# Kernel optimization log

Measured on AMD Instinct MI355X. Metric: run time of the kernel, lower is better.

The kernel has to match this reference:

```python
import jax, jax.numpy as jnp
import numpy as np

HEAD_NUM = 12
HEAD_SIZE = 64
INPUT_DIM = 768
BATCH = 2
SEQ = 2048
NEG = 1e12


def setup_inputs() -> dict:
    key = jax.random.key(0)
    k1, k2, k3 = jax.random.split(key, 3)
    x = jax.random.normal(k1, (BATCH, SEQ, INPUT_DIM), dtype=jnp.float32)
    W = jax.random.normal(k2, (INPUT_DIM, HEAD_NUM * HEAD_SIZE * 2), dtype=jnp.float32) * 0.02
    b = jax.random.normal(k3, (HEAD_NUM * HEAD_SIZE * 2,), dtype=jnp.float32) * 0.02
    mask = jnp.ones((BATCH, SEQ), dtype=jnp.int32)
    return {"x": x, "W": W, "b": b, "mask": mask}


def _rope_tables(n, d, dtype):
    # SinusoidalPositionEmbedding(head_size, 'zero'): pos[..., 0::2]=sin, 1::2=cos
    pos = jnp.arange(n, dtype=dtype)
    freqs = jnp.power(10000.0, -2.0 * jnp.arange(d // 2, dtype=dtype) / d)
    ang = pos[:, None] * freqs[None, :]  # [n, d/2]
    # K.repeat_elements(pos[..., 1::2], 2, -1) -> each cos value repeated twice
    cos_pos = jnp.repeat(jnp.cos(ang), 2, axis=-1)  # [n, d]
    sin_pos = jnp.repeat(jnp.sin(ang), 2, axis=-1)  # [n, d]
    return cos_pos[None, :, None, :], sin_pos[None, :, None, :]  # [1,n,1,d]


def _rotate_half(t):
    # stack([-t[...,1::2], t[...,::2]], -1).reshape(t.shape)
    t2 = jnp.stack([-t[..., 1::2], t[..., 0::2]], axis=-1)
    return t2.reshape(t.shape)


def reference(x, W, b, mask):
    bsz, n, _ = x.shape
    proj = (x @ W + b).reshape(bsz, n, HEAD_NUM, 2 * HEAD_SIZE)  # [b,n,h,2d]
    qw, kw = proj[..., :HEAD_SIZE], proj[..., HEAD_SIZE:]
    cos_pos, sin_pos = _rope_tables(n, HEAD_SIZE, x.dtype)
    qw = qw * cos_pos + _rotate_half(qw) * sin_pos
    kw = kw * cos_pos + _rotate_half(kw) * sin_pos
    logits = jnp.einsum('bmhd,bnhd->bhmn', qw, kw)  # [b,h,m,n]
    m = mask.astype(logits.dtype)
    logits = logits - (1.0 - m[:, None, :, None]) * NEG  # mask query axis (dim 2)
    logits = logits - (1.0 - m[:, None, None, :]) * NEG  # mask key axis (dim 3)
    tri = jnp.triu(jnp.ones((n, n), dtype=logits.dtype))  # band_part(0,-1): keep m<=n
    logits = logits - (1.0 - tri) * NEG
    return logits / (HEAD_SIZE ** 0.5)
```

## Files before the change

kernel.cpp:

```cpp
#include <hip/hip_runtime.h>

#define SEQ    2048
#define IND    768
#define NPROJ  1536
#define BHN    24
#define NEGV   1000000000000.0f

typedef __attribute__((ext_vector_type(4))) float f32x4;
typedef __attribute__((ext_vector_type(8))) short s16x8;
typedef __attribute__((ext_vector_type(8))) unsigned short u16x8;
typedef __attribute__((ext_vector_type(4))) unsigned short u16x4;

__device__ __forceinline__ unsigned short f2bf(float f) {
  unsigned int u = __builtin_bit_cast(unsigned int, f);
  u += 0x7fffu + ((u >> 16) & 1u);
  return (unsigned short)(u >> 16);
}

__device__ __forceinline__ void nt_store4(float* p, f32x4 v) {
  __builtin_nontemporal_store(v, (f32x4*)p);
}

#define GLOAD_LDS16(g, l)                                              \
  __builtin_amdgcn_global_load_lds(                                    \
      (const __attribute__((address_space(1))) void*)(g),              \
      (__attribute__((address_space(3))) void*)(l), 16, 0, 0)

__device__ __forceinline__ void stage128x64(const unsigned short* __restrict__ src,
                                            size_t stride, int4* lds, int tid) {
  const int w = tid >> 6, l = tid & 63;
#pragma unroll
  for (int i = 0; i < 4; ++i) {
    int gb = w * 256 + i * 64;
    int G = gb + l;
    int row = G >> 3, g = G & 7;
    int cb = g ^ (row & 7);
    GLOAD_LDS16(src + (size_t)row * stride + cb * 8, lds + gb);
  }
}

__global__ __launch_bounds__(256) void k_prep(const float* __restrict__ x,
                                              const float* __restrict__ W,
                                              unsigned short* __restrict__ xb,
                                              unsigned short* __restrict__ Wt,
                                              float* __restrict__ cosT,
                                              float* __restrict__ sinT) {
  __shared__ float Ws[64][65];
  const int bid = blockIdx.x;
  const int tid = threadIdx.x;

  if (bid < 1536) {
    int i = (bid * 256 + tid) * 8;
    float4 a = *(const float4*)(x + i);
    float4 b = *(const float4*)(x + i + 4);
    u16x8 o;
    o[0] = f2bf(a.x); o[1] = f2bf(a.y); o[2] = f2bf(a.z); o[3] = f2bf(a.w);
    o[4] = f2bf(b.x); o[5] = f2bf(b.y); o[6] = f2bf(b.z); o[7] = f2bf(b.w);
    *(u16x8*)(xb + i) = o;
  } else if (bid < 1824) {
    int tb = bid - 1536;
    int nt = tb % 24, kt = tb / 24;
    int n0 = nt * 64, k0 = kt * 64;
    int cr = tid >> 4;
    int cc = (tid & 15) * 4;
#pragma unroll
    for (int it = 0; it < 4; ++it) {
      int kr = it * 16 + cr;
      float4 v = *(const float4*)(W + (size_t)(k0 + kr) * NPROJ + n0 + cc);
      Ws[kr][cc + 0] = v.x; Ws[kr][cc + 1] = v.y;
      Ws[kr][cc + 2] = v.z; Ws[kr][cc + 3] = v.w;
    }
    __syncthreads();
#pragma unroll
    for (int it = 0; it < 4; ++it) {
      int nl = it * 16 + cr;
      u16x4 o;
#pragma unroll
      for (int q = 0; q < 4; ++q) o[q] = f2bf(Ws[cc + q][nl]);
      *(u16x4*)(Wt + (size_t)(n0 + nl) * IND + k0 + cc) = o;
    }
  } else {
    int i = (bid - 1824) * 256 + tid;
    int s = i >> 5, f = i & 31;
    float freq = exp2f(-(float)f * (13.287712379549449f / 32.0f));
    float ang = (float)s * freq;
    float sv, cv;
    sincosf(ang, &sv, &cv);
    cosT[i] = cv; sinT[i] = sv;
  }
}

__global__ __launch_bounds__(256, 2) void k_proj(const unsigned short* __restrict__ xb,
                                                 const unsigned short* __restrict__ Wt,
                                                 const float* __restrict__ bias,
                                                 unsigned short* __restrict__ Qb,
                                                 unsigned short* __restrict__ Kb,
                                                 const float* __restrict__ cosT,
                                                 const float* __restrict__ sinT) {
  __shared__ int4 As4[2][1024];
  __shared__ int4 Bs4[2][1024];
  const int tid = threadIdx.x;
  const int bidl = blockIdx.x;
  const int bid = (bidl & 7) * 48 + (bidl >> 3);
  const int nt = bid % 12, mt = bid / 12;
  const int m0 = mt * 128, n0 = nt * 128;
  const int wid = tid >> 6, lane = tid & 63;
  const int wr = wid >> 1, wc = wid & 1;
  const int lr = lane & 15, kg = lane >> 4;

  f32x4 acc[4][4] = {};

  const unsigned short* Abase = xb + (size_t)m0 * IND;
  const unsigned short* Bbase = Wt + (size_t)n0 * IND;

  stage128x64(Abase, IND, As4[0], tid);
  stage128x64(Bbase, IND, Bs4[0], tid);
  __syncthreads();

  for (int kt = 0; kt < 12; ++kt) {
    int cur = kt & 1;
    if (kt < 11) {
      stage128x64(Abase + (kt + 1) * 64, IND, As4[cur ^ 1], tid);
      stage128x64(Bbase + (kt + 1) * 64, IND, Bs4[cur ^ 1], tid);
    }
    const int4* Ac = As4[cur];
    const int4* Bc = Bs4[cur];
#pragma unroll
    for (int kk = 0; kk < 2; ++kk) {
      s16x8 af[4], bfr[4];
#pragma unroll
      for (int i = 0; i < 4; ++i) {
        int r = wr * 64 + i * 16 + lr;
        af[i] = *(const s16x8*)&Ac[r * 8 + ((kk * 4 + kg) ^ (r & 7))];
      }
#pragma unroll
      for (int j = 0; j < 4; ++j) {
        int r = wc * 64 + j * 16 + lr;
        bfr[j] = *(const s16x8*)&Bc[r * 8 + ((kk * 4 + kg) ^ (r & 7))];
      }
#pragma unroll
      for (int i = 0; i < 4; ++i)
#pragma unroll
        for (int j = 0; j < 4; ++j)
          acc[i][j] = __builtin_amdgcn_mfma_f32_16x16x32_bf16(af[i], bfr[j], acc[i][j], 0, 0, 0);
    }
    __syncthreads();
  }

#pragma unroll
  for (int i = 0; i < 4; ++i) {
    int rowb = m0 + wr * 64 + i * 16 + kg * 4;
#pragma unroll
    for (int j = 0; j < 4; ++j) {
      int col = n0 + wc * 64 + j * 16 + lr;
      float bcol = bias[col];
      int d = col & 63;
      int h = col >> 7;
      bool isq = (col & 64) == 0;
      unsigned short* dst = isq ? Qb : Kb;
#pragma unroll
      for (int r = 0; r < 4; ++r) {
        int m = rowb + r;
        int s = m & (SEQ - 1), bb = m >> 11;
        float v = acc[i][j][r] + bcol;
        float p = __shfl_xor(v, 1);
        int ti = s * 32 + (d >> 1);
        float cv = cosT[ti], sv = sinT[ti];
        float o = (col & 1) ? (v * cv + p * sv) : (v * cv - p * sv);
        dst[((size_t)(bb * 12 + h) * SEQ + s) * 64 + d] = f2bf(o);
      }
    }
  }
}

__global__ __launch_bounds__(256, 4) void k_attn(const unsigned short* __restrict__ Qb,
                                                 const unsigned short* __restrict__ Kb,
                                                 const int* __restrict__ mask,
                                                 float* __restrict__ out) {
  __shared__ int4 smem[2048];
  int4* Qs4 = smem;
  int4* Ks4 = smem + 1024;

  const int b0 = blockIdx.x;
  const int lin = (b0 & 7) * 768 + (b0 >> 3);
  const int bh = lin >> 8;
  const int rem = lin & 255;
  const int mt = rem >> 4, nt = rem & 15;
  const int b = bh / 12;
  const int tid = threadIdx.x;
  const int m0 = mt * 128, n0 = nt * 128;
  const float scale = 0.125f;

  if (nt < mt) {
#pragma unroll
    for (int it = 0; it < 16; ++it) {
      int id = it * 256 + tid;
      int row = id >> 5, c4 = id & 31;
      int gm = m0 + row;
      float rm = (float)mask[b * SEQ + gm];
      int gn0 = n0 + c4 * 4;
      f32x4 v;
#pragma unroll
      for (int q = 0; q < 4; ++q) {
        float cm = (float)mask[b * SEQ + gn0 + q];
        v[q] = -(NEGV * ((1.f - rm) + (1.f - cm) + 1.f)) * scale;
      }
      nt_store4(out + ((size_t)bh * SEQ + gm) * SEQ + gn0, v);
    }
    return;
  }

  const int wid = tid >> 6, lane = tid & 63;
  const int wr = wid >> 1, wc = wid & 1;
  const int lr = lane & 15, kg = lane >> 4;

  stage128x64(Qb + ((size_t)bh * SEQ + m0) * 64, 64, Qs4, tid);
  stage128x64(Kb + ((size_t)bh * SEQ + n0) * 64, 64, Ks4, tid);
  __syncthreads();

  f32x4 acc[4][4] = {};
#pragma unroll
  for (int kk = 0; kk < 2; ++kk) {
    s16x8 af[4], bfr[4];
#pragma unroll
    for (int i = 0; i < 4; ++i) {
      int r = wr * 64 + i * 16 + lr;
      af[i] = *(const s16x8*)&Qs4[r * 8 + ((kk * 4 + kg) ^ (r & 7))];
    }
#pragma unroll
    for (int j = 0; j < 4; ++j) {
      int r = wc * 64 + j * 16 + lr;
      bfr[j] = *(const s16x8*)&Ks4[r * 8 + ((kk * 4 + kg) ^ (r & 7))];
    }
#pragma unroll
    for (int i = 0; i < 4; ++i)
#pragma unroll
      for (int j = 0; j < 4; ++j)
        acc[i][j] = __builtin_amdgcn_mfma_f32_16x16x32_bf16(af[i], bfr[j], acc[i][j], 0, 0, 0);
  }

  __syncthreads();
  float* Cs = (float*)smem;

#pragma unroll
  for (int c = 0; c < 2; ++c) {
    if (wr == c) {
#pragma unroll
      for (int i = 0; i < 4; ++i)
#pragma unroll
        for (int j = 0; j < 4; ++j) {
          int col = wc * 64 + j * 16 + lr;
          int g = col >> 2;
#pragma unroll
          for (int r = 0; r < 4; ++r) {
            int rl = i * 16 + kg * 4 + r;
            int gs = g ^ (rl & 7);
            Cs[rl * 128 + gs * 4 + (col & 3)] = acc[i][j][r];
          }
        }
    }
    __syncthreads();
#pragma unroll
    for (int it = 0; it < 8; ++it) {
      int id = it * 256 + tid;
      int rl = id >> 5, g = id & 31;
      int gs = g ^ (rl & 7);
      f32x4 v = *(const f32x4*)&Cs[rl * 128 + gs * 4];
      int gm = m0 + c * 64 + rl;
      int gn0 = n0 + g * 4;
      float rmv = (float)mask[b * SEQ + gm];
      int4 cm = *(const int4*)&mask[b * SEQ + gn0];
      f32x4 o;
#pragma unroll
      for (int q = 0; q < 4; ++q) {
        int gn = gn0 + q;
        float cmv = (float)((const int*)&cm)[q];
        float pen = (1.f - rmv) + (1.f - cmv) + ((gn < gm) ? 1.f : 0.f);
        o[q] = (v[q] - NEGV * pen) * scale;
      }
      nt_store4(out + ((size_t)bh * SEQ + gm) * SEQ + gn0, o);
    }
    __syncthreads();
  }
}

extern "C" void kernel_launch(void* const* d_in, const int* in_sizes, int n_in,
                              void* d_out, int out_size, void* d_ws, size_t ws_size,
                              hipStream_t stream) {
  const float* x    = (const float*)d_in[0];
  const float* W    = (const float*)d_in[1];
  const float* bias = (const float*)d_in[2];
  const int*   mask = (const int*)d_in[3];
  float* out = (float*)d_out;

  char* ws = (char*)d_ws;
  unsigned short* xb = (unsigned short*)(ws);
  unsigned short* Wt = (unsigned short*)(ws + 6291456);
  unsigned short* Qb = (unsigned short*)(ws + 6291456 + 2359296);
  unsigned short* Kb = (unsigned short*)(ws + 6291456 + 2359296 + 6291456);
  float* cosT = (float*)(ws + 6291456 + 2359296 + 6291456 + 6291456);
  float* sinT = (float*)(ws + 6291456 + 2359296 + 6291456 + 6291456 + 262144);

  k_prep<<<2080, 256, 0, stream>>>(x, W, xb, Wt, cosT, sinT);
  k_proj<<<384, 256, 0, stream>>>(xb, Wt, bias, Qb, Kb, cosT, sinT);
  k_attn<<<6144, 256, 0, stream>>>(Qb, Kb, mask, out);
}
```

Before: 103.1 us.

## Fuse masked-tile fill into projection kernel and stage Q/K stores through LDS

```diff
diff --git a/kernel.cpp b/kernel.cpp
--- a/kernel.cpp
+++ b/kernel.cpp
@@ -90,16 +90,48 @@
   }
 }
 
-__global__ __launch_bounds__(256, 2) void k_proj(const unsigned short* __restrict__ xb,
-                                                 const unsigned short* __restrict__ Wt,
-                                                 const float* __restrict__ bias,
-                                                 unsigned short* __restrict__ Qb,
-                                                 unsigned short* __restrict__ Kb,
-                                                 const float* __restrict__ cosT,
-                                                 const float* __restrict__ sinT) {
-  __shared__ int4 As4[2][1024];
-  __shared__ int4 Bs4[2][1024];
+__global__ __launch_bounds__(256, 2) void k_projfill(const unsigned short* __restrict__ xb,
+                                                     const unsigned short* __restrict__ Wt,
+                                                     const float* __restrict__ bias,
+                                                     unsigned short* __restrict__ Qb,
+                                                     unsigned short* __restrict__ Kb,
+                                                     const float* __restrict__ cosT,
+                                                     const float* __restrict__ sinT,
+                                                     const int* __restrict__ mask,
+                                                     float* __restrict__ out) {
+  __shared__ int4 smem2[4096];
   const int tid = threadIdx.x;
+
+  if (blockIdx.x >= 384) {
+    int fid = blockIdx.x - 384;
+    int bh = fid / 120;
+    int t = fid - bh * 120;
+    int mt = 1;
+    while (t >= mt) { t -= mt; ++mt; }
+    int nt = t;
+    int b = bh / 12;
+    int m0 = mt * 128, n0 = nt * 128;
+    const float scale = 0.125f;
+#pragma unroll
+    for (int it = 0; it < 16; ++it) {
+      int id = it * 256 + tid;
+      int row = id >> 5, c4 = id & 31;
+      int gm = m0 + row;
+      float rm = (float)mask[b * SEQ + gm];
+      int gn0 = n0 + c4 * 4;
+      f32x4 v;
+#pragma unroll
+      for (int q = 0; q < 4; ++q) {
+        float cm = (float)mask[b * SEQ + gn0 + q];
+        v[q] = -(NEGV * ((1.f - rm) + (1.f - cm) + 1.f)) * scale;
+      }
+      nt_store4(out + ((size_t)bh * SEQ + gm) * SEQ + gn0, v);
+    }
+    return;
+  }
+
+  int4* As4 = smem2;
+  int4* Bs4 = smem2 + 2048;
   const int bidl = blockIdx.x;
   const int bid = (bidl & 7) * 48 + (bidl >> 3);
   const int nt = bid % 12, mt = bid / 12;
@@ -113,18 +145,18 @@
   const unsigned short* Abase = xb + (size_t)m0 * IND;
   const unsigned short* Bbase = Wt + (size_t)n0 * IND;
 
-  stage128x64(Abase, IND, As4[0], tid);
-  stage128x64(Bbase, IND, Bs4[0], tid);
+  stage128x64(Abase, IND, As4, tid);
+  stage128x64(Bbase, IND, Bs4, tid);
   __syncthreads();
 
   for (int kt = 0; kt < 12; ++kt) {
     int cur = kt & 1;
     if (kt < 11) {
-      stage128x64(Abase + (kt + 1) * 64, IND, As4[cur ^ 1], tid);
-      stage128x64(Bbase + (kt + 1) * 64, IND, Bs4[cur ^ 1], tid);
-    }
-    const int4* Ac = As4[cur];
-    const int4* Bc = Bs4[cur];
+      stage128x64(Abase + (kt + 1) * 64, IND, As4 + (cur ^ 1) * 1024, tid);
+      stage128x64(Bbase + (kt + 1) * 64, IND, Bs4 + (cur ^ 1) * 1024, tid);
+    }
+    const int4* Ac = As4 + cur * 1024;
+    const int4* Bc = Bs4 + cur * 1024;
 #pragma unroll
     for (int kk = 0; kk < 2; ++kk) {
       s16x8 af[4], bfr[4];
@@ -147,29 +179,43 @@
     __syncthreads();
   }
 
+  unsigned short* Cs = (unsigned short*)As4;
 #pragma unroll
   for (int i = 0; i < 4; ++i) {
-    int rowb = m0 + wr * 64 + i * 16 + kg * 4;
 #pragma unroll
     for (int j = 0; j < 4; ++j) {
-      int col = n0 + wc * 64 + j * 16 + lr;
+      int colr = wc * 64 + j * 16 + lr;
+      int col = n0 + colr;
       float bcol = bias[col];
       int d = col & 63;
-      int h = col >> 7;
-      bool isq = (col & 64) == 0;
-      unsigned short* dst = isq ? Qb : Kb;
 #pragma unroll
       for (int r = 0; r < 4; ++r) {
-        int m = rowb + r;
-        int s = m & (SEQ - 1), bb = m >> 11;
+        int rowr = wr * 64 + i * 16 + kg * 4 + r;
+        int s = (m0 + rowr) & (SEQ - 1);
         float v = acc[i][j][r] + bcol;
         float p = __shfl_xor(v, 1);
         int ti = s * 32 + (d >> 1);
         float cv = cosT[ti], sv = sinT[ti];
         float o = (col & 1) ? (v * cv + p * sv) : (v * cv - p * sv);
-        dst[((size_t)(bb * 12 + h) * SEQ + s) * 64 + d] = f2bf(o);
-      }
-    }
+        int gs = (colr >> 3) ^ (rowr & 15);
+        Cs[rowr * 128 + gs * 8 + (colr & 7)] = f2bf(o);
+      }
+    }
+  }
+  __syncthreads();
+#pragma unroll
+  for (int it = 0; it < 8; ++it) {
+    int id = it * 256 + tid;
+    int rowr = id >> 4, g = id & 15;
+    int gs = g ^ (rowr & 15);
+    u16x8 v = *(const u16x8*)&Cs[rowr * 128 + gs * 8];
+    int m = m0 + rowr;
+    int s = m & (SEQ - 1), bb = m >> 11;
+    int colg = n0 + g * 8;
+    int h = colg >> 7;
+    int d0 = colg & 63;
+    unsigned short* dst = ((colg & 64) == 0) ? Qb : Kb;
+    *(u16x8*)(dst + ((size_t)(bb * 12 + h) * SEQ + s) * 64 + d0) = v;
   }
 }
 
@@ -182,33 +228,16 @@
   int4* Ks4 = smem + 1024;
 
   const int b0 = blockIdx.x;
-  const int lin = (b0 & 7) * 768 + (b0 >> 3);
-  const int bh = lin >> 8;
-  const int rem = lin & 255;
-  const int mt = rem >> 4, nt = rem & 15;
+  const int lin = (b0 & 7) * 408 + (b0 >> 3);
+  int bh = lin / 136;
+  int t = lin - bh * 136;
+  int mt = 0;
+  while (t >= 16 - mt) { t -= 16 - mt; ++mt; }
+  const int nt = mt + t;
   const int b = bh / 12;
   const int tid = threadIdx.x;
   const int m0 = mt * 128, n0 = nt * 128;
   const float scale = 0.125f;
-
-  if (nt < mt) {
-#pragma unroll
-    for (int it = 0; it < 16; ++it) {
-      int id = it * 256 + tid;
-      int row = id >> 5, c4 = id & 31;
-      int gm = m0 + row;
-      float rm = (float)mask[b * SEQ + gm];
-      int gn0 = n0 + c4 * 4;
-      f32x4 v;
-#pragma unroll
-      for (int q = 0; q < 4; ++q) {
-        float cm = (float)mask[b * SEQ + gn0 + q];
-        v[q] = -(NEGV * ((1.f - rm) + (1.f - cm) + 1.f)) * scale;
-      }
-      nt_store4(out + ((size_t)bh * SEQ + gm) * SEQ + gn0, v);
-    }
-    return;
-  }
 
   const int wid = tid >> 6, lane = tid & 63;
   const int wr = wid >> 1, wc = wid & 1;
@@ -302,6 +331,6 @@
   float* sinT = (float*)(ws + 6291456 + 2359296 + 6291456 + 6291456 + 262144);
 
   k_prep<<<2080, 256, 0, stream>>>(x, W, xb, Wt, cosT, sinT);
-  k_proj<<<384, 256, 0, stream>>>(xb, Wt, bias, Qb, Kb, cosT, sinT);
-  k_attn<<<6144, 256, 0, stream>>>(Qb, Kb, mask, out);
-}
+  k_projfill<<<3264, 256, 0, stream>>>(xb, Wt, bias, Qb, Kb, cosT, sinT, mask, out);
+  k_attn<<<3264, 256, 0, stream>>>(Qb, Kb, mask, out);
+}
```

Result: faster. 98.73 us (-4.2%).
